# Kernel tuning notes

Hardware: AMD Instinct MI355X
Metric: run time of the kernel (lower is better)

## Reference

```python
import jax, jax.numpy as jnp
import numpy as np

HEADS = 8
HID = 128
N_A = 10000
N_B = 10000
E = 120000
NG = 8  # graphs in batch
F_A = 256
F_B = 128
NEG_SLOPE = 0.2


def _gat(h_src, h_dst, src, dst, ws, wd, a_s, a_d, bias, num_dst):
    """PyG GATConv, bipartite, concat=False, add_self_loops=False."""
    hs = (h_src @ ws).reshape(-1, HEADS, HID)   # [N_src, H, C]
    hd = (h_dst @ wd).reshape(-1, HEADS, HID)   # [N_dst, H, C]
    al_s = jnp.sum(hs * a_s, axis=-1)           # [N_src, H]
    al_d = jnp.sum(hd * a_d, axis=-1)           # [N_dst, H]
    e = jax.nn.leaky_relu(al_s[src] + al_d[dst], NEG_SLOPE)  # [E, H]
    m = jax.ops.segment_max(e, dst, num_segments=num_dst)
    ex = jnp.exp(e - m[dst])
    denom = jax.ops.segment_sum(ex, dst, num_segments=num_dst)
    alpha = ex / (denom[dst] + 1e-16)           # segment softmax over in-edges
    msg = hs[src] * alpha[:, :, None]           # [E, H, C]
    out = jax.ops.segment_sum(msg, dst, num_segments=num_dst)
    return out.mean(axis=1) + bias              # concat=False -> head mean + bias


def _mean_pool(x, batch, num_graphs):
    s = jax.ops.segment_sum(x, batch, num_segments=num_graphs)
    cnt = jax.ops.segment_sum(jnp.ones((x.shape[0],), x.dtype), batch, num_segments=num_graphs)
    return s / jnp.maximum(cnt, 1.0)[:, None]


def setup_inputs() -> dict:
    key = jax.random.key(0)
    ks = iter(jax.random.split(key, 48))
    rn = lambda shape, s=0.05: jax.random.normal(next(ks), shape, jnp.float32) * s
    inp = {
        'x_a': jax.random.normal(next(ks), (N_A, F_A), jnp.float32),
        'x_b': jax.random.normal(next(ks), (N_B, F_B), jnp.float32),
        'edge_ab': jax.random.randint(next(ks), (2, E), 0, N_A, jnp.int32),
        'edge_ba': jax.random.randint(next(ks), (2, E), 0, N_B, jnp.int32),
        'batch_a': jnp.sort(jax.random.randint(next(ks), (N_A,), 0, NG, jnp.int32)),
        'batch_b': jnp.sort(jax.random.randint(next(ks), (N_B,), 0, NG, jnp.int32)),
        'lin_a_w': rn((F_A, HID)), 'lin_a_b': rn((HID,)),
        'lin_b_w': rn((F_B, HID)), 'lin_b_b': rn((HID,)),
        'fc_w': rn((2 * HID, 1)), 'fc_b': rn((1,)),
    }
    for layer in ('1', '2'):
        for rel in ('ab', 'ba'):
            inp[f'w{layer}s_{rel}'] = rn((HID, HEADS * HID))
            inp[f'w{layer}d_{rel}'] = rn((HID, HEADS * HID))
            inp[f'a{layer}s_{rel}'] = rn((HEADS, HID))
            inp[f'a{layer}d_{rel}'] = rn((HEADS, HID))
            inp[f'b{layer}_{rel}'] = rn((HID,))
    return inp


def reference(x_a, x_b, edge_ab, edge_ba, batch_a, batch_b,
              lin_a_w, lin_a_b, lin_b_w, lin_b_b, fc_w, fc_b,
              w1s_ab, w1d_ab, a1s_ab, a1d_ab, b1_ab,
              w1s_ba, w1d_ba, a1s_ba, a1d_ba, b1_ba,
              w2s_ab, w2d_ab, a2s_ab, a2d_ab, b2_ab,
              w2s_ba, w2d_ba, a2s_ba, a2d_ba, b2_ba):
    ha = jax.nn.relu(x_a @ lin_a_w + lin_a_b)
    hb = jax.nn.relu(x_b @ lin_b_w + lin_b_b)
    # layer 1 (each dst type receives exactly one relation -> HeteroConv mean is identity)
    hb1 = _gat(ha, hb, edge_ab[0], edge_ab[1], w1s_ab, w1d_ab, a1s_ab, a1d_ab, b1_ab, N_B)
    ha1 = _gat(hb, ha, edge_ba[0], edge_ba[1], w1s_ba, w1d_ba, a1s_ba, a1d_ba, b1_ba, N_A)
    ha1 = jax.nn.relu(ha1)
    hb1 = jax.nn.relu(hb1)
    # layer 2
    hb2 = _gat(ha1, hb1, edge_ab[0], edge_ab[1], w2s_ab, w2d_ab, a2s_ab, a2d_ab, b2_ab, N_B)
    ha2 = _gat(hb1, ha1, edge_ba[0], edge_ba[1], w2s_ba, w2d_ba, a2s_ba, a2d_ba, b2_ba, N_A)
    pa = _mean_pool(ha2, batch_a, NG)
    pb = _mean_pool(hb2, batch_b, NG)
    g = jnp.concatenate([pa, pb], axis=1)       # [NG, 2*HID]
    return (g @ fc_w + fc_b).squeeze(-1)        # [NG]
```

## Files before the change

### kernel.cpp

```cpp
#include <hip/hip_runtime.h>
#include <math.h>

#define HID 128
#define HEADS 8

typedef __attribute__((ext_vector_type(8))) short s16x8;
typedef __attribute__((ext_vector_type(4))) float f32x4;

__device__ __forceinline__ unsigned short bf16_rne(float x) {
  unsigned u = __float_as_uint(x);
  unsigned r = u + 0x7FFFu + ((u >> 16) & 1u);
  return (unsigned short)(r >> 16);
}
__device__ __forceinline__ float bf16f(unsigned short h) {
  return __uint_as_float(((unsigned)h) << 16);
}

struct PrepArgs {
  const float* W[8];
  const float* a[8];
  unsigned short* WThi[4];
  unsigned short* WTlo[4];
  float* v[8];
};
struct PrepX {
  const float* lwa; const float* lwb;
  unsigned short *wa_hi, *wa_lo, *wb_hi, *wb_lo;
  int KA, KB, nwa, nwb;
};

__global__ __launch_bounds__(256) void prep_hist(
    PrepArgs p, PrepX px,
    const int* __restrict__ dst_ab, const int* __restrict__ dst_ba,
    int* __restrict__ cnt_ab, int* __restrict__ cnt_ba, int E)
{
  int bid = blockIdx.x;
  if (bid < 2048) {
    int g = bid >> 9;
    int idx = ((bid & 511) << 8) + threadIdx.x;
    int kidx = idx & 1023;
    int c = idx >> 10;
    int h = kidx >> 7, k = kidx & 127;
    float wv = p.W[2 * g][(size_t)k * (HEADS * HID) + h * HID + c];
    unsigned short hi = bf16_rne(wv);
    unsigned short lo = bf16_rne(wv - bf16f(hi));
    p.WThi[g][idx] = hi;
    p.WTlo[g][idx] = lo;
  } else if (bid < 2080) {
    int u = bid - 2048;
    int wi = u >> 2;
    int gid = ((u & 3) << 8) + threadIdx.x;
    int k = gid >> 3, h = gid & 7;
    const float* wr = p.W[wi] + (size_t)k * (HEADS * HID) + h * HID;
    const float* ar = p.a[wi] + (size_t)h * HID;
    float s = 0.f;
    for (int c = 0; c < HID; c++) s = fmaf(wr[c], ar[c], s);
    p.v[wi][gid] = s;
  } else if (bid < 2080 + px.nwa) {
    int idx = (bid - 2080) * 256 + threadIdx.x;
    if (idx < px.KA * HID) {
      int k = idx % px.KA, c = idx / px.KA;
      float wv = px.lwa[(size_t)k * HID + c];
      unsigned short hi = bf16_rne(wv);
      unsigned short lo = bf16_rne(wv - bf16f(hi));
      px.wa_hi[idx] = hi;
      px.wa_lo[idx] = lo;
    }
  } else if (bid < 2080 + px.nwa + px.nwb) {
    int idx = (bid - 2080 - px.nwa) * 256 + threadIdx.x;
    if (idx < px.KB * HID) {
      int k = idx % px.KB, c = idx / px.KB;
      float wv = px.lwb[(size_t)k * HID + c];
      unsigned short hi = bf16_rne(wv);
      unsigned short lo = bf16_rne(wv - bf16f(hi));
      px.wb_hi[idx] = hi;
      px.wb_lo[idx] = lo;
    }
  } else {
    int gid = (bid - 2080 - px.nwa - px.nwb) * 256 + threadIdx.x;
    if (gid < E) atomicAdd(&cnt_ab[dst_ab[gid]], 1);
    else if (gid < 2 * E) atomicAdd(&cnt_ba[dst_ba[gid - E]], 1);
  }
}

__global__ __launch_bounds__(1024) void scan2(
    const int* __restrict__ cnt_ab, const int* __restrict__ cnt_ba,
    int* __restrict__ ip_ab, int* __restrict__ ip_ba, int n_ab, int n_ba)
{
  const int* cnt = (blockIdx.x == 0) ? cnt_ab : cnt_ba;
  int* indptr = (blockIdx.x == 0) ? ip_ab : ip_ba;
  int n = (blockIdx.x == 0) ? n_ab : n_ba;
  __shared__ int parts[1024];
  const int tid = threadIdx.x;
  const int base = tid * 10;
  int local[10];
  int s = 0;
#pragma unroll
  for (int j = 0; j < 10; j++) {
    int v = (base + j < n) ? cnt[base + j] : 0;
    local[j] = v; s += v;
  }
  parts[tid] = s;
  __syncthreads();
  for (int off = 1; off < 1024; off <<= 1) {
    int v = (tid >= off) ? parts[tid - off] : 0;
    __syncthreads();
    parts[tid] += v;
    __syncthreads();
  }
  int ex = parts[tid] - s;
#pragma unroll
  for (int j = 0; j < 10; j++) {
    if (base + j < n) indptr[base + j] = ex;
    ex += local[j];
  }
  if (tid == 1023) indptr[n] = parts[1023];
}

__global__ __launch_bounds__(256) void scatter2(
    const int* __restrict__ edge_ab, const int* __restrict__ edge_ba,
    const int* __restrict__ ip_ab, const int* __restrict__ ip_ba,
    int* __restrict__ cur_ab, int* __restrict__ cur_ba,
    int* __restrict__ srcs_ab, int* __restrict__ srcs_ba, int E)
{
  int gid = blockIdx.x * 256 + threadIdx.x;
  if (gid < E) {
    int d = edge_ab[E + gid];
    int pos = ip_ab[d] + atomicAdd(&cur_ab[d], 1);
    srcs_ab[pos] = edge_ab[gid];
  } else if (gid < 2 * E) {
    int g = gid - E;
    int d = edge_ba[E + g];
    int pos = ip_ba[d] + atomicAdd(&cur_ba[d], 1);
    srcs_ba[pos] = edge_ba[g];
  }
}

struct ISeg {
  const float* A;
  const unsigned short* Bhi; const unsigned short* Blo;
  float* out; const float* bias; int M; int K; int yb;
};

__global__ __launch_bounds__(256) void gemm_mfma_in(ISeg s0, ISeg s1)
{
  __shared__ __align__(16) unsigned short smem[12288];
  const int tid = threadIdx.x;
  const float* A; const unsigned short *Bhi, *Blo; const float* bias; float* out;
  int M, K, ytile;
  if ((int)blockIdx.x < s0.yb) {
    A = s0.A; Bhi = s0.Bhi; Blo = s0.Blo; out = s0.out; bias = s0.bias;
    M = s0.M; K = s0.K; ytile = blockIdx.x;
  } else {
    A = s1.A; Bhi = s1.Bhi; Blo = s1.Blo; out = s1.out; bias = s1.bias;
    M = s1.M; K = s1.K; ytile = blockIdx.x - s0.yb;
  }
  const int bm = ytile * 64;
  const int nks = K >> 5;

  const int sr = tid >> 2;
  const int sg = tid & 3;
  const int g1 = sg ^ ((sr >> 1) & 3);
  const int sr2 = sr + 64;
  const int g2 = sg ^ ((sr2 >> 1) & 3);
  const int aslot  = sr * 32 + g1 * 8;
  const int bslotA = sr * 32 + g1 * 8;
  const int bslotB = sr2 * 32 + g2 * 8;
  const int gr = bm + sr;
  const bool arow_ok = (gr < M);
  const float* gA = A + (size_t)gr * K + sg * 8;
  const unsigned short* gB0 = Bhi + (size_t)sr  * K + sg * 8;
  const unsigned short* gB1 = Bhi + (size_t)sr2 * K + sg * 8;
  const unsigned short* gC0 = Blo + (size_t)sr  * K + sg * 8;
  const unsigned short* gC1 = Blo + (size_t)sr2 * K + sg * 8;

  const int l = tid & 63;
  const int w = tid >> 6;
  const int kg = l >> 4;
  int aoff[4], boff[2];
#pragma unroll
  for (int mi = 0; mi < 4; mi++) {
    int r = mi * 16 + (l & 15);
    aoff[mi] = r * 32 + (kg ^ ((r >> 1) & 3)) * 8;
  }
#pragma unroll
  for (int ni = 0; ni < 2; ni++) {
    int r = w * 32 + ni * 16 + (l & 15);
    boff[ni] = r * 32 + (kg ^ ((r >> 1) & 3)) * 8;
  }

  f32x4 acc[4][2];
  const f32x4 z4 = {0.f, 0.f, 0.f, 0.f};
#pragma unroll
  for (int mi = 0; mi < 4; mi++)
#pragma unroll
    for (int ni = 0; ni < 2; ni++) acc[mi][ni] = z4;

  float4 fa0 = make_float4(0.f, 0.f, 0.f, 0.f), fa1 = fa0;
  if (arow_ok) { fa0 = *(const float4*)gA; fa1 = *(const float4*)(gA + 4); }
  uint4 rB0 = *(const uint4*)gB0;
  uint4 rB1 = *(const uint4*)gB1;
  uint4 rC0 = *(const uint4*)gC0;
  uint4 rC1 = *(const uint4*)gC1;

  for (int ks = 0; ks < nks; ks++) {
    {
      const float f[8] = {fa0.x, fa0.y, fa0.z, fa0.w, fa1.x, fa1.y, fa1.z, fa1.w};
      unsigned au[4], lu[4];
#pragma unroll
      for (int i = 0; i < 4; i++) {
        unsigned short h0 = bf16_rne(f[2 * i]);
        unsigned short l0 = bf16_rne(f[2 * i] - bf16f(h0));
        unsigned short h1 = bf16_rne(f[2 * i + 1]);
        unsigned short l1 = bf16_rne(f[2 * i + 1] - bf16f(h1));
        au[i] = (unsigned)h0 | ((unsigned)h1 << 16);
        lu[i] = (unsigned)l0 | ((unsigned)l1 << 16);
      }
      *(uint4*)&smem[aslot]        = make_uint4(au[0], au[1], au[2], au[3]);
      *(uint4*)&smem[2048 + aslot] = make_uint4(lu[0], lu[1], lu[2], lu[3]);
    }
    *(uint4*)&smem[4096 + bslotA] = rB0;
    *(uint4*)&smem[4096 + bslotB] = rB1;
    *(uint4*)&smem[8192 + bslotA] = rC0;
    *(uint4*)&smem[8192 + bslotB] = rC1;
    __syncthreads();
    if (ks < nks - 1) {
      const int k0 = (ks + 1) * 32;
      if (arow_ok) {
        fa0 = *(const float4*)(gA + k0);
        fa1 = *(const float4*)(gA + k0 + 4);
      }
      rB0 = *(const uint4*)(gB0 + k0);
      rB1 = *(const uint4*)(gB1 + k0);
      rC0 = *(const uint4*)(gC0 + k0);
      rC1 = *(const uint4*)(gC1 + k0);
    }
    s16x8 bh0 = *(const s16x8*)&smem[4096 + boff[0]];
    s16x8 bh1 = *(const s16x8*)&smem[4096 + boff[1]];
    s16x8 bl0 = *(const s16x8*)&smem[8192 + boff[0]];
    s16x8 bl1 = *(const s16x8*)&smem[8192 + boff[1]];
#pragma unroll
    for (int mi = 0; mi < 4; mi++) {
      s16x8 ah = *(const s16x8*)&smem[aoff[mi]];
      s16x8 al = *(const s16x8*)&smem[2048 + aoff[mi]];
      acc[mi][0] = __builtin_amdgcn_mfma_f32_16x16x32_bf16(ah, bh0, acc[mi][0], 0, 0, 0);
      acc[mi][1] = __builtin_amdgcn_mfma_f32_16x16x32_bf16(ah, bh1, acc[mi][1], 0, 0, 0);
      acc[mi][0] = __builtin_amdgcn_mfma_f32_16x16x32_bf16(ah, bl0, acc[mi][0], 0, 0, 0);
      acc[mi][1] = __builtin_amdgcn_mfma_f32_16x16x32_bf16(ah, bl1, acc[mi][1], 0, 0, 0);
      acc[mi][0] = __builtin_amdgcn_mfma_f32_16x16x32_bf16(al, bh0, acc[mi][0], 0, 0, 0);
      acc[mi][1] = __builtin_amdgcn_mfma_f32_16x16x32_bf16(al, bh1, acc[mi][1], 0, 0, 0);
      acc[mi][0] = __builtin_amdgcn_mfma_f32_16x16x32_bf16(al, bl0, acc[mi][0], 0, 0, 0);
      acc[mi][1] = __builtin_amdgcn_mfma_f32_16x16x32_bf16(al, bl1, acc[mi][1], 0, 0, 0);
    }
    __syncthreads();
  }

  const int q = l >> 4, cl = l & 15;
#pragma unroll
  for (int ni = 0; ni < 2; ni++) {
    const int col = w * 32 + ni * 16 + cl;
    const float bv = bias[col];
#pragma unroll
    for (int mi = 0; mi < 4; mi++) {
      const int r0 = bm + mi * 16 + q * 4;
      const f32x4 v = acc[mi][ni];
#pragma unroll
      for (int j = 0; j < 4; j++) {
        const int r = r0 + j;
        if (r < M) {
          float x = v[j] + bv;
          x = fmaxf(x, 0.f);
          out[(size_t)r * HID + col] = x;
        }
      }
    }
  }
}

__global__ __launch_bounds__(256) void compute_al4(
    const float* __restrict__ ha, const float* __restrict__ hb,
    const float* __restrict__ v4,
    float* __restrict__ o0, float* __restrict__ o1,
    float* __restrict__ o2, float* __restrict__ o3, int na, int nb)
{
  __shared__ float vsh[4 * HID * HEADS];
  for (int i = threadIdx.x; i < 4 * HID * HEADS; i += 256) vsh[i] = v4[i];
  __syncthreads();
  int gid = blockIdx.x * 256 + threadIdx.x;
  int row = gid >> 3, h = gid & 7;
  const float* hr; float* o; int q, rl;
  if (row < na)                    { q = 0; rl = row;               hr = ha; o = o0; }
  else if (row < na + nb)          { q = 1; rl = row - na;          hr = hb; o = o1; }
  else if (row < na + 2 * nb)      { q = 2; rl = row - na - nb;     hr = hb; o = o2; }
  else if (row < 2 * na + 2 * nb)  { q = 3; rl = row - na - 2 * nb; hr = ha; o = o3; }
  else return;
  hr += (size_t)rl * HID;
  const float* vq = vsh + q * HID * HEADS;
  float s = 0.f;
  for (int k = 0; k < HID; k++) s = fmaf(hr[k], vq[k * HEADS + h], s);
  o[(size_t)rl * HEADS + h] = s;
}

struct GDir {
  const int* indptr; const int* srcs;
  const float* als; const float* ald;
  const float* h;
  unsigned short* zhi; unsigned short* zlo;
};

__global__ __launch_bounds__(256) void gat_edge2(GDir d0, GDir d1, int n0, int ntot)
{
  const int w = threadIdx.x >> 6;
  const int lane = threadIdx.x & 63;
  const int g = blockIdx.x * 4 + w;
  if (g >= ntot) return;
  const bool first = (g < n0);
  const int n = first ? g : g - n0;
  const int* indptr = first ? d0.indptr : d1.indptr;
  const int* srcs   = first ? d0.srcs   : d1.srcs;
  const float* als  = first ? d0.als    : d1.als;
  const float* ald  = first ? d0.ald    : d1.ald;
  const float* hsrc = first ? d0.h      : d1.h;
  unsigned short* zh = (first ? d0.zhi : d1.zhi) + (size_t)n * (HEADS * HID);
  unsigned short* zl = (first ? d0.zlo : d1.zlo) + (size_t)n * (HEADS * HID);

  const int base = indptr[n];
  const int deg = indptr[n + 1] - base;
  if (deg == 0) {
#pragma unroll
    for (int hh = 0; hh < HEADS; hh++) {
      *(unsigned*)(zh + hh * HID + 2 * lane) = 0u;
      *(unsigned*)(zl + hh * HID + 2 * lane) = 0u;
    }
    return;
  }
  const int eh = lane >> 3, h = lane & 7;
  const float aldn = ald[(size_t)n * HEADS + h];
  const int nch = (deg + 7) >> 3;
  const int ncc = nch < 4 ? nch : 4;

  int sc[4];
  float vc[4];
#pragma unroll
  for (int c = 0; c < 4; c++) {
    int e = c * 8 + eh;
    sc[c] = (c < ncc && e < deg) ? srcs[base + e] : -1;
  }
#pragma unroll
  for (int c = 0; c < 4; c++)
    vc[c] = (sc[c] >= 0) ? als[(size_t)sc[c] * HEADS + h] : 0.f;
  float den = 0.f;
#pragma unroll
  for (int c = 0; c < 4; c++) {
    float v = vc[c] + aldn;
    v = v > 0.f ? v : 0.2f * v;
    float ex = (sc[c] >= 0) ? expf(v) : 0.f;
    vc[c] = ex;
    den += ex;
  }
  for (int e0 = 32; e0 < deg; e0 += 8) {
    int e = e0 + eh;
    if (e < deg) {
      int s = srcs[base + e];
      float v = als[(size_t)s * HEADS + h] + aldn;
      v = v > 0.f ? v : 0.2f * v;
      den += expf(v);
    }
  }
  den += __shfl_xor(den, 8);
  den += __shfl_xor(den, 16);
  den += __shfl_xor(den, 32);

  float acc[16];
#pragma unroll
  for (int i = 0; i < 16; i++) acc[i] = 0.f;
#pragma unroll
  for (int c = 0; c < 4; c++) {
    if (c >= ncc) break;
    const int rem = deg - c * 8;
    const int elim = rem < 8 ? rem : 8;
#pragma unroll
    for (int half = 0; half < 2; half++) {
      if (half * 4 >= elim) break;
      int sj[4];
#pragma unroll
      for (int j = 0; j < 4; j++) {
        int s = __shfl(sc[c], (half * 4 + j) * 8);
        sj[j] = s < 0 ? 0 : s;
      }
      float2 hv[4];
#pragma unroll
      for (int j = 0; j < 4; j++)
        hv[j] = *(const float2*)(hsrc + (size_t)sj[j] * HID + 2 * lane);
#pragma unroll
      for (int j = 0; j < 4; j++) {
#pragma unroll
        for (int hh = 0; hh < 8; hh++) {
          float a = __shfl(vc[c], (half * 4 + j) * 8 + hh);
          acc[2 * hh]     = fmaf(a, hv[j].x, acc[2 * hh]);
          acc[2 * hh + 1] = fmaf(a, hv[j].y, acc[2 * hh + 1]);
        }
      }
    }
  }
  for (int e0 = 32; e0 < deg; e0 += 8) {
    int e = e0 + eh;
    int s = (e < deg) ? srcs[base + e] : -1;
    float ex = 0.f;
    if (s >= 0) {
      float v = als[(size_t)s * HEADS + h] + aldn;
      v = v > 0.f ? v : 0.2f * v;
      ex = expf(v);
    }
    int elim = deg - e0; if (elim > 8) elim = 8;
    for (int e8 = 0; e8 < elim; e8++) {
      int ss = __shfl(s, e8 * 8);
      const float2 hvt = *(const float2*)(hsrc + (size_t)ss * HID + 2 * lane);
#pragma unroll
      for (int hh = 0; hh < 8; hh++) {
        float a = __shfl(ex, e8 * 8 + hh);
        acc[2 * hh]     = fmaf(a, hvt.x, acc[2 * hh]);
        acc[2 * hh + 1] = fmaf(a, hvt.y, acc[2 * hh + 1]);
      }
    }
  }
#pragma unroll
  for (int hh = 0; hh < 8; hh++) {
    float dh = __shfl(den, hh);
    float inv = 1.f / (dh + 1e-16f);
    float x0 = acc[2 * hh] * inv;
    float x1 = acc[2 * hh + 1] * inv;
    unsigned short h0 = bf16_rne(x0), h1 = bf16_rne(x1);
    unsigned short l0 = bf16_rne(x0 - bf16f(h0)), l1 = bf16_rne(x1 - bf16f(h1));
    *(unsigned*)(zh + hh * HID + 2 * lane) = (unsigned)h0 | ((unsigned)h1 << 16);
    *(unsigned*)(zl + hh * HID + 2 * lane) = (unsigned)l0 | ((unsigned)l1 << 16);
  }
}

struct MSeg {
  const unsigned short* Ahi; const unsigned short* Alo;
  const unsigned short* Bhi; const unsigned short* Blo;
  float* out; const float* bias; int M; int yb;
};

__global__ __launch_bounds__(512) void gemm_mfma8(MSeg s0, MSeg s1, float scale, int do_relu)
{
  __shared__ __align__(16) unsigned short smem[24576];
  const int tid = threadIdx.x;
  const unsigned short *Ahi, *Alo, *Bhi, *Blo; const float* bias; float* out; int M, ytile;
  if ((int)blockIdx.x < s0.yb) {
    Ahi = s0.Ahi; Alo = s0.Alo; Bhi = s0.Bhi; Blo = s0.Blo;
    out = s0.out; bias = s0.bias; M = s0.M; ytile = blockIdx.x;
  } else {
    Ahi = s1.Ahi; Alo = s1.Alo; Bhi = s1.Bhi; Blo = s1.Blo;
    out = s1.out; bias = s1.bias; M = s1.M; ytile = blockIdx.x - s0.yb;
  }
  const int bm = ytile * 64;
  const int half = tid >> 8;
  const int t = tid & 255;
  const int kbase = half * 512;
  unsigned short* sm = smem + half * 12288;

  const int sr = t >> 2;
  const int sg = t & 3;
  const int g1 = sg ^ ((sr >> 1) & 3);
  const int sr2 = sr + 64;
  const int g2 = sg ^ ((sr2 >> 1) & 3);
  const int aslot  = sr * 32 + g1 * 8;
  const int bslotA = sr * 32 + g1 * 8;
  const int bslotB = sr2 * 32 + g2 * 8;
  const unsigned short* gA  = Ahi + (size_t)(bm + sr) * 1024 + kbase + sg * 8;
  const unsigned short* gAl = Alo + (size_t)(bm + sr) * 1024 + kbase + sg * 8;
  const unsigned short* gB0 = Bhi + (size_t)sr  * 1024 + kbase + sg * 8;
  const unsigned short* gB1 = Bhi + (size_t)sr2 * 1024 + kbase + sg * 8;
  const unsigned short* gC0 = Blo + (size_t)sr  * 1024 + kbase + sg * 8;
  const unsigned short* gC1 = Blo + (size_t)sr2 * 1024 + kbase + sg * 8;

  const int l = t & 63;
  const int w = t >> 6;
  const int kg = l >> 4;
  int aoff[4], boff[2];
#pragma unroll
  for (int mi = 0; mi < 4; mi++) {
    int r = mi * 16 + (l & 15);
    aoff[mi] = r * 32 + (kg ^ ((r >> 1) & 3)) * 8;
  }
#pragma unroll
  for (int ni = 0; ni < 2; ni++) {
    int r = w * 32 + ni * 16 + (l & 15);
    boff[ni] = r * 32 + (kg ^ ((r >> 1) & 3)) * 8;
  }

  f32x4 acc[4][2];
  const f32x4 z4 = {0.f, 0.f, 0.f, 0.f};
#pragma unroll
  for (int mi = 0; mi < 4; mi++)
#pragma unroll
    for (int ni = 0; ni < 2; ni++) acc[mi][ni] = z4;

  uint4 rA  = *(const uint4*)gA;
  uint4 rAl = *(const uint4*)gAl;
  uint4 rB0 = *(const uint4*)gB0;
  uint4 rB1 = *(const uint4*)gB1;
  uint4 rC0 = *(const uint4*)gC0;
  uint4 rC1 = *(const uint4*)gC1;

  for (int ks = 0; ks < 16; ks++) {
    *(uint4*)&sm[aslot]         = rA;
    *(uint4*)&sm[2048 + aslot]  = rAl;
    *(uint4*)&sm[4096 + bslotA] = rB0;
    *(uint4*)&sm[4096 + bslotB] = rB1;
    *(uint4*)&sm[8192 + bslotA] = rC0;
    *(uint4*)&sm[8192 + bslotB] = rC1;
    __syncthreads();
    if (ks < 15) {
      const int k0 = (ks + 1) * 32;
      rA  = *(const uint4*)(gA  + k0);
      rAl = *(const uint4*)(gAl + k0);
      rB0 = *(const uint4*)(gB0 + k0);
      rB1 = *(const uint4*)(gB1 + k0);
      rC0 = *(const uint4*)(gC0 + k0);
      rC1 = *(const uint4*)(gC1 + k0);
    }
    s16x8 bh0 = *(const s16x8*)&sm[4096 + boff[0]];
    s16x8 bh1 = *(const s16x8*)&sm[4096 + boff[1]];
    s16x8 bl0 = *(const s16x8*)&sm[8192 + boff[0]];
    s16x8 bl1 = *(const s16x8*)&sm[8192 + boff[1]];
#pragma unroll
    for (int mi = 0; mi < 4; mi++) {
      s16x8 ah = *(const s16x8*)&sm[aoff[mi]];
      s16x8 al = *(const s16x8*)&sm[2048 + aoff[mi]];
      acc[mi][0] = __builtin_amdgcn_mfma_f32_16x16x32_bf16(ah, bh0, acc[mi][0], 0, 0, 0);
      acc[mi][1] = __builtin_amdgcn_mfma_f32_16x16x32_bf16(ah, bh1, acc[mi][1], 0, 0, 0);
      acc[mi][0] = __builtin_amdgcn_mfma_f32_16x16x32_bf16(ah, bl0, acc[mi][0], 0, 0, 0);
      acc[mi][1] = __builtin_amdgcn_mfma_f32_16x16x32_bf16(ah, bl1, acc[mi][1], 0, 0, 0);
      acc[mi][0] = __builtin_amdgcn_mfma_f32_16x16x32_bf16(al, bh0, acc[mi][0], 0, 0, 0);
      acc[mi][1] = __builtin_amdgcn_mfma_f32_16x16x32_bf16(al, bh1, acc[mi][1], 0, 0, 0);
      acc[mi][0] = __builtin_amdgcn_mfma_f32_16x16x32_bf16(al, bl0, acc[mi][0], 0, 0, 0);
      acc[mi][1] = __builtin_amdgcn_mfma_f32_16x16x32_bf16(al, bl1, acc[mi][1], 0, 0, 0);
    }
    __syncthreads();
  }

  float* fred = (float*)smem;
  const int q = l >> 4, cl = l & 15;
  if (half == 1) {
#pragma unroll
    for (int ni = 0; ni < 2; ni++) {
      const int col = w * 32 + ni * 16 + cl;
#pragma unroll
      for (int mi = 0; mi < 4; mi++) {
        const f32x4 v = acc[mi][ni];
#pragma unroll
        for (int j = 0; j < 4; j++)
          fred[(mi * 16 + q * 4 + j) * 128 + col] = v[j];
      }
    }
  }
  __syncthreads();
  if (half == 0) {
#pragma unroll
    for (int ni = 0; ni < 2; ni++) {
      const int col = w * 32 + ni * 16 + cl;
      const float bv = bias[col];
#pragma unroll
      for (int mi = 0; mi < 4; mi++) {
        const int rt = mi * 16 + q * 4;
        const f32x4 v = acc[mi][ni];
#pragma unroll
        for (int j = 0; j < 4; j++) {
          const int r = bm + rt + j;
          if (r < M) {
            float x = (v[j] + fred[(rt + j) * 128 + col]) * scale + bv;
            if (do_relu) x = fmaxf(x, 0.f);
            out[(size_t)r * HID + col] = x;
          }
        }
      }
    }
  }
}

__global__ __launch_bounds__(256) void pool_fin(
    const float* __restrict__ ha, const float* __restrict__ hb,
    const int* __restrict__ batch_a, const int* __restrict__ batch_b,
    const float* __restrict__ fc_w, const float* __restrict__ fc_b,
    float* __restrict__ gsum, int* __restrict__ ticket,
    float* __restrict__ out, int na, int nb, int ng)
{
  const bool isA = blockIdx.x < 160;
  const float* h = isA ? ha : hb;
  const int* batch = isA ? batch_a : batch_b;
  const float* wseg = isA ? fc_w : fc_w + HID;
  float* gs = isA ? gsum : gsum + 8;
  const int n = isA ? na : nb;
  const int b = isA ? blockIdx.x : blockIdx.x - 160;

  __shared__ float sg[8];
  __shared__ int lastf;
  if (threadIdx.x < 8) sg[threadIdx.x] = 0.f;
  __syncthreads();
  const int lane = threadIdx.x & 63;
  const int wv = threadIdx.x >> 6;
  const int gw = b * 4 + wv;
  const int tw = 160 * 4;
  const float2 w2 = *(const float2*)(wseg + lane * 2);
  for (int r = gw; r < n; r += tw) {
    float2 hv = *(const float2*)(h + (size_t)r * HID + lane * 2);
    float s = hv.x * w2.x + hv.y * w2.y;
#pragma unroll
    for (int off = 32; off > 0; off >>= 1) s += __shfl_down(s, off, 64);
    if (lane == 0) atomicAdd(&sg[batch[r]], s);
  }
  __syncthreads();
  if (threadIdx.x < 8) atomicAdd(&gs[threadIdx.x], sg[threadIdx.x]);
  if (threadIdx.x == 0) {
    __threadfence();
    int tk = atomicAdd(ticket, 1);
    lastf = (tk == (int)gridDim.x - 1);
  }
  __syncthreads();
  if (lastf) {
    int g = threadIdx.x;
    if (g < ng) {
      int l, r, lo;
      l = 0; r = na; while (l < r) { int m = (l + r) >> 1; if (batch_a[m] < g) l = m + 1; else r = m; } lo = l;
      r = na; while (l < r) { int m = (l + r) >> 1; if (batch_a[m] < g + 1) l = m + 1; else r = m; }
      int ca = l - lo; if (ca < 1) ca = 1;
      l = 0; r = nb; while (l < r) { int m = (l + r) >> 1; if (batch_b[m] < g) l = m + 1; else r = m; } lo = l;
      r = nb; while (l < r) { int m = (l + r) >> 1; if (batch_b[m] < g + 1) l = m + 1; else r = m; }
      int cb = l - lo; if (cb < 1) cb = 1;
      float va = atomicAdd(&gsum[g], 0.f);
      float vb = atomicAdd(&gsum[8 + g], 0.f);
      out[g] = va / (float)ca + vb / (float)cb + fc_b[0];
    }
  }
}

extern "C" void kernel_launch(void* const* d_in, const int* in_sizes, int n_in,
                              void* d_out, int out_size, void* d_ws, size_t ws_size,
                              hipStream_t stream)
{
  const float* x_a = (const float*)d_in[0];
  const float* x_b = (const float*)d_in[1];
  const int* edge_ab = (const int*)d_in[2];
  const int* edge_ba = (const int*)d_in[3];
  const int* batch_a = (const int*)d_in[4];
  const int* batch_b = (const int*)d_in[5];
  const float* lin_a_w = (const float*)d_in[6];
  const float* lin_a_b = (const float*)d_in[7];
  const float* lin_b_w = (const float*)d_in[8];
  const float* lin_b_b = (const float*)d_in[9];
  const float* fc_w = (const float*)d_in[10];
  const float* fc_b = (const float*)d_in[11];

  const int NA = in_sizes[4];
  const int NB = in_sizes[5];
  const int E  = in_sizes[2] / 2;
  const int FA = in_sizes[0] / NA;
  const int FB = in_sizes[1] / NB;
  const int NG = out_size;
  const int NMAX = NA > NB ? NA : NB;
  const int NAp = (NA + 127) & ~127, NBp = (NB + 127) & ~127;
  const int NMAXp = NAp > NBp ? NAp : NBp;

  auto al256 = [](size_t b) { return (b + 255) & ~(size_t)255; };
  size_t fixed = 0;
  fixed += 3 * al256((size_t)NAp * HID * 4) + 3 * al256((size_t)NBp * HID * 4);
  fixed += 2 * al256((size_t)NMAXp * 1024 * 2);
  fixed += al256((size_t)8 * 131072 * 2);
  fixed += 2 * al256((size_t)FA * HID * 2) + 2 * al256((size_t)FB * HID * 2);
  fixed += al256((size_t)8 * HID * HEADS * 4);
  fixed += 2 * al256((size_t)NAp * HEADS * 4) + 2 * al256((size_t)NBp * HEADS * 4);
  fixed += al256(((size_t)4 * NMAX + 24) * 4);
  fixed += al256((size_t)(NB + 1) * 4) + al256((size_t)(NA + 1) * 4);
  fixed += 2 * al256((size_t)E * 4);
  fixed += 8192;
  const size_t zba_sz = 2 * al256((size_t)NAp * 1024 * 2);

  bool dual = (fixed + zba_sz <= ws_size);
  if (fixed > ws_size) return;

  char* w = (char*)d_ws;
  auto carve = [&](size_t bytes) -> void* {
    void* p = (void*)w;
    w += (bytes + 255) & ~(size_t)255;
    return p;
  };
  float* ha0 = (float*)carve((size_t)NAp * HID * 4);
  float* hb0 = (float*)carve((size_t)NBp * HID * 4);
  float* ha1 = (float*)carve((size_t)NAp * HID * 4);
  float* hb1 = (float*)carve((size_t)NBp * HID * 4);
  float* ha2 = (float*)carve((size_t)NAp * HID * 4);
  float* hb2 = (float*)carve((size_t)NBp * HID * 4);
  unsigned short* zab_hi = (unsigned short*)carve((size_t)NMAXp * 1024 * 2);
  unsigned short* zab_lo = (unsigned short*)carve((size_t)NMAXp * 1024 * 2);
  unsigned short* zba_hi = dual ? (unsigned short*)carve((size_t)NAp * 1024 * 2) : zab_hi;
  unsigned short* zba_lo = dual ? (unsigned short*)carve((size_t)NAp * 1024 * 2) : zab_lo;
  unsigned short* WT = (unsigned short*)carve((size_t)8 * 131072 * 2);
  unsigned short* wa_hi = (unsigned short*)carve((size_t)FA * HID * 2);
  unsigned short* wa_lo = (unsigned short*)carve((size_t)FA * HID * 2);
  unsigned short* wb_hi = (unsigned short*)carve((size_t)FB * HID * 2);
  unsigned short* wb_lo = (unsigned short*)carve((size_t)FB * HID * 2);
  float* vv  = (float*)carve((size_t)8 * HID * HEADS * 4);
  float* als_ab = (float*)carve((size_t)NAp * HEADS * 4);
  float* ald_ab = (float*)carve((size_t)NBp * HEADS * 4);
  float* als_ba = (float*)carve((size_t)NBp * HEADS * 4);
  float* ald_ba = (float*)carve((size_t)NAp * HEADS * 4);
  int* csrblk = (int*)carve(((size_t)4 * NMAX + 24) * 4);
  int* indptr_ab = (int*)carve((size_t)(NB + 1) * 4);
  int* indptr_ba = (int*)carve((size_t)(NA + 1) * 4);
  int* srcs_ab   = (int*)carve((size_t)E * 4);
  int* srcs_ba   = (int*)carve((size_t)E * 4);
  if ((size_t)(w - (char*)d_ws) > ws_size) return;

  int* cnt_ab = csrblk;
  int* cnt_ba = csrblk + NMAX;
  int* cur_ab = csrblk + 2 * NMAX;
  int* cur_ba = csrblk + 3 * NMAX;
  float* gsum = (float*)(csrblk + 4 * NMAX);
  int* ticket = csrblk + 4 * NMAX + 16;

  hipMemsetAsync(csrblk, 0, ((size_t)4 * NMAX + 24) * 4, stream);

  PrepArgs pa;
  const int wi_idx[8] = {12, 13, 17, 18, 22, 23, 27, 28};
  const int ai_idx[8] = {14, 15, 19, 20, 24, 25, 29, 30};
  for (int i = 0; i < 8; i++) {
    pa.W[i] = (const float*)d_in[wi_idx[i]];
    pa.a[i] = (const float*)d_in[ai_idx[i]];
    pa.v[i] = vv + (size_t)i * HID * HEADS;
  }
  for (int g = 0; g < 4; g++) {
    pa.WThi[g] = WT + (size_t)g * 131072;
    pa.WTlo[g] = WT + (size_t)(4 + g) * 131072;
  }
  PrepX px;
  px.lwa = lin_a_w; px.lwb = lin_b_w;
  px.wa_hi = wa_hi; px.wa_lo = wa_lo; px.wb_hi = wb_hi; px.wb_lo = wb_lo;
  px.KA = FA; px.KB = FB;
  px.nwa = (FA * HID + 255) / 256;
  px.nwb = (FB * HID + 255) / 256;
  const int hist_b = (2 * E + 255) / 256;
  prep_hist<<<2080 + px.nwa + px.nwb + hist_b, 256, 0, stream>>>(
      pa, px, edge_ab + E, edge_ba + E, cnt_ab, cnt_ba, E);
  scan2<<<2, 1024, 0, stream>>>(cnt_ab, cnt_ba, indptr_ab, indptr_ba, NB, NA);
  scatter2<<<(2 * E + 255) / 256, 256, 0, stream>>>(
      edge_ab, edge_ba, indptr_ab, indptr_ba, cur_ab, cur_ba, srcs_ab, srcs_ba, E);

  {
    ISeg sa = {x_a, wa_hi, wa_lo, ha0, lin_a_b, NA, FA, NAp / 64};
    ISeg sb = {x_b, wb_hi, wb_lo, hb0, lin_b_b, NB, FB, NBp / 64};
    gemm_mfma_in<<<NAp / 64 + NBp / 64, 256, 0, stream>>>(sa, sb);
  }

  auto run_layer = [&](int L, const float* haP, const float* hbP,
                       float* haN, float* hbN, const float* b_ab, const float* b_ba,
                       int relu) {
    compute_al4<<<((2 * (NA + NB)) * HEADS + 255) / 256, 256, 0, stream>>>(
        haP, hbP, vv + (size_t)L * 4 * HID * HEADS,
        als_ab, ald_ab, als_ba, ald_ba, NA, NB);
    GDir dab = {indptr_ab, srcs_ab, als_ab, ald_ab, haP, zab_hi, zab_lo};
    GDir dba = {indptr_ba, srcs_ba, als_ba, ald_ba, hbP, zba_hi, zba_lo};
    const int gab = 2 * L, gba = 2 * L + 1;
    MSeg mab = {zab_hi, zab_lo, WT + (size_t)gab * 131072, WT + (size_t)(4 + gab) * 131072,
                hbN, b_ab, NB, NBp / 64};
    MSeg mba = {zba_hi, zba_lo, WT + (size_t)gba * 131072, WT + (size_t)(4 + gba) * 131072,
                haN, b_ba, NA, NAp / 64};
    if (dual) {
      gat_edge2<<<(NB + NA + 3) / 4, 256, 0, stream>>>(dab, dba, NB, NB + NA);
      gemm_mfma8<<<NBp / 64 + NAp / 64, 512, 0, stream>>>(mab, mba, 1.f / HEADS, relu);
    } else {
      MSeg mz = {nullptr, nullptr, nullptr, nullptr, nullptr, nullptr, 0, 0};
      gat_edge2<<<(NB + 3) / 4, 256, 0, stream>>>(dab, dab, NB, NB);
      gemm_mfma8<<<NBp / 64, 512, 0, stream>>>(mab, mz, 1.f / HEADS, relu);
      gat_edge2<<<(NA + 3) / 4, 256, 0, stream>>>(dba, dba, NA, NA);
      gemm_mfma8<<<NAp / 64, 512, 0, stream>>>(mba, mz, 1.f / HEADS, relu);
    }
  };

  run_layer(0, ha0, hb0, ha1, hb1, (const float*)d_in[16], (const float*)d_in[21], 1);
  run_layer(1, ha1, hb1, ha2, hb2, (const float*)d_in[26], (const float*)d_in[31], 0);

  pool_fin<<<320, 256, 0, stream>>>(ha2, hb2, batch_a, batch_b, fc_w, fc_b,
                                    gsum, ticket, (float*)d_out, NA, NB, NG);
}
```

Baseline: 371.9 us.

## Split the post-aggregation GEMM along K with a separate reduce-and-epilogue kernel

The fused 512-thread GEMM, which split K in two halves inside a block and reduced through shared memory, becomes a 256-thread split-K kernel. It uses a grid dimension of KS (up to 4) slices that write fp32 partials to a workspace buffer, and a new reduce_epi kernel sums the partials and applies scale, bias and ReLU. The aim is more blocks in flight and better occupancy, since the old grid had only about 320 blocks. The cost is an extra kernel launch per layer plus the round trip of the partials through global memory, and the workspace requirement grows, so the code now picks KS based on available workspace.

```diff
diff --git a/kernel.cpp b/kernel.cpp
--- a/kernel.cpp
+++ b/kernel.cpp
@@ -440,44 +440,44 @@
 struct MSeg {
   const unsigned short* Ahi; const unsigned short* Alo;
   const unsigned short* Bhi; const unsigned short* Blo;
-  float* out; const float* bias; int M; int yb;
+  int M; int yb;
 };
 
-__global__ __launch_bounds__(512) void gemm_mfma8(MSeg s0, MSeg s1, float scale, int do_relu)
-{
-  __shared__ __align__(16) unsigned short smem[24576];
+__global__ __launch_bounds__(256, 2) void gemm_mfma_splitk(
+    MSeg s0, MSeg s1, float* __restrict__ P, int Mtot, int KS)
+{
+  __shared__ __align__(16) unsigned short smem[12288];
   const int tid = threadIdx.x;
-  const unsigned short *Ahi, *Alo, *Bhi, *Blo; const float* bias; float* out; int M, ytile;
+  const unsigned short *Ahi, *Alo, *Bhi, *Blo; int M, ytile, rowbase;
   if ((int)blockIdx.x < s0.yb) {
     Ahi = s0.Ahi; Alo = s0.Alo; Bhi = s0.Bhi; Blo = s0.Blo;
-    out = s0.out; bias = s0.bias; M = s0.M; ytile = blockIdx.x;
+    M = s0.M; ytile = blockIdx.x; rowbase = 0;
   } else {
     Ahi = s1.Ahi; Alo = s1.Alo; Bhi = s1.Bhi; Blo = s1.Blo;
-    out = s1.out; bias = s1.bias; M = s1.M; ytile = blockIdx.x - s0.yb;
+    M = s1.M; ytile = blockIdx.x - s0.yb; rowbase = s0.yb * 64;
   }
   const int bm = ytile * 64;
-  const int half = tid >> 8;
-  const int t = tid & 255;
-  const int kbase = half * 512;
-  unsigned short* sm = smem + half * 12288;
-
-  const int sr = t >> 2;
-  const int sg = t & 3;
+  const int kchunk = 1024 / KS;
+  const int kbeg = blockIdx.y * kchunk;
+  const int nks = kchunk / 32;
+
+  const int sr = tid >> 2;
+  const int sg = tid & 3;
   const int g1 = sg ^ ((sr >> 1) & 3);
   const int sr2 = sr + 64;
   const int g2 = sg ^ ((sr2 >> 1) & 3);
   const int aslot  = sr * 32 + g1 * 8;
   const int bslotA = sr * 32 + g1 * 8;
   const int bslotB = sr2 * 32 + g2 * 8;
-  const unsigned short* gA  = Ahi + (size_t)(bm + sr) * 1024 + kbase + sg * 8;
-  const unsigned short* gAl = Alo + (size_t)(bm + sr) * 1024 + kbase + sg * 8;
-  const unsigned short* gB0 = Bhi + (size_t)sr  * 1024 + kbase + sg * 8;
-  const unsigned short* gB1 = Bhi + (size_t)sr2 * 1024 + kbase + sg * 8;
-  const unsigned short* gC0 = Blo + (size_t)sr  * 1024 + kbase + sg * 8;
-  const unsigned short* gC1 = Blo + (size_t)sr2 * 1024 + kbase + sg * 8;
-
-  const int l = t & 63;
-  const int w = t >> 6;
+  const unsigned short* gA  = Ahi + (size_t)(bm + sr) * 1024 + kbeg + sg * 8;
+  const unsigned short* gAl = Alo + (size_t)(bm + sr) * 1024 + kbeg + sg * 8;
+  const unsigned short* gB0 = Bhi + (size_t)sr  * 1024 + kbeg + sg * 8;
+  const unsigned short* gB1 = Bhi + (size_t)sr2 * 1024 + kbeg + sg * 8;
+  const unsigned short* gC0 = Blo + (size_t)sr  * 1024 + kbeg + sg * 8;
+  const unsigned short* gC1 = Blo + (size_t)sr2 * 1024 + kbeg + sg * 8;
+
+  const int l = tid & 63;
+  const int w = tid >> 6;
   const int kg = l >> 4;
   int aoff[4], boff[2];
 #pragma unroll
@@ -505,15 +505,15 @@
   uint4 rC0 = *(const uint4*)gC0;
   uint4 rC1 = *(const uint4*)gC1;
 
-  for (int ks = 0; ks < 16; ks++) {
-    *(uint4*)&sm[aslot]         = rA;
-    *(uint4*)&sm[2048 + aslot]  = rAl;
-    *(uint4*)&sm[4096 + bslotA] = rB0;
-    *(uint4*)&sm[4096 + bslotB] = rB1;
-    *(uint4*)&sm[8192 + bslotA] = rC0;
-    *(uint4*)&sm[8192 + bslotB] = rC1;
+  for (int ks = 0; ks < nks; ks++) {
+    *(uint4*)&smem[aslot]         = rA;
+    *(uint4*)&smem[2048 + aslot]  = rAl;
+    *(uint4*)&smem[4096 + bslotA] = rB0;
+    *(uint4*)&smem[4096 + bslotB] = rB1;
+    *(uint4*)&smem[8192 + bslotA] = rC0;
+    *(uint4*)&smem[8192 + bslotB] = rC1;
     __syncthreads();
-    if (ks < 15) {
+    if (ks < nks - 1) {
       const int k0 = (ks + 1) * 32;
       rA  = *(const uint4*)(gA  + k0);
       rAl = *(const uint4*)(gAl + k0);
@@ -522,14 +522,14 @@
       rC0 = *(const uint4*)(gC0 + k0);
       rC1 = *(const uint4*)(gC1 + k0);
     }
-    s16x8 bh0 = *(const s16x8*)&sm[4096 + boff[0]];
-    s16x8 bh1 = *(const s16x8*)&sm[4096 + boff[1]];
-    s16x8 bl0 = *(const s16x8*)&sm[8192 + boff[0]];
-    s16x8 bl1 = *(const s16x8*)&sm[8192 + boff[1]];
+    s16x8 bh0 = *(const s16x8*)&smem[4096 + boff[0]];
+    s16x8 bh1 = *(const s16x8*)&smem[4096 + boff[1]];
+    s16x8 bl0 = *(const s16x8*)&smem[8192 + boff[0]];
+    s16x8 bl1 = *(const s16x8*)&smem[8192 + boff[1]];
 #pragma unroll
     for (int mi = 0; mi < 4; mi++) {
-      s16x8 ah = *(const s16x8*)&sm[aoff[mi]];
-      s16x8 al = *(const s16x8*)&sm[2048 + aoff[mi]];
+      s16x8 ah = *(const s16x8*)&smem[aoff[mi]];
+      s16x8 al = *(const s16x8*)&smem[2048 + aoff[mi]];
       acc[mi][0] = __builtin_amdgcn_mfma_f32_16x16x32_bf16(ah, bh0, acc[mi][0], 0, 0, 0);
       acc[mi][1] = __builtin_amdgcn_mfma_f32_16x16x32_bf16(ah, bh1, acc[mi][1], 0, 0, 0);
       acc[mi][0] = __builtin_amdgcn_mfma_f32_16x16x32_bf16(ah, bl0, acc[mi][0], 0, 0, 0);
@@ -542,43 +542,57 @@
     __syncthreads();
   }
 
-  float* fred = (float*)smem;
   const int q = l >> 4, cl = l & 15;
-  if (half == 1) {
-#pragma unroll
-    for (int ni = 0; ni < 2; ni++) {
-      const int col = w * 32 + ni * 16 + cl;
-#pragma unroll
-      for (int mi = 0; mi < 4; mi++) {
-        const f32x4 v = acc[mi][ni];
-#pragma unroll
-        for (int j = 0; j < 4; j++)
-          fred[(mi * 16 + q * 4 + j) * 128 + col] = v[j];
+  const size_t prow0 = (size_t)blockIdx.y * Mtot + rowbase + bm;
+#pragma unroll
+  for (int ni = 0; ni < 2; ni++) {
+    const int col = w * 32 + ni * 16 + cl;
+#pragma unroll
+    for (int mi = 0; mi < 4; mi++) {
+      const int r0 = mi * 16 + q * 4;
+      const f32x4 v = acc[mi][ni];
+#pragma unroll
+      for (int j = 0; j < 4; j++) {
+        const int r = r0 + j;
+        if (bm + r < M) P[(prow0 + r) * HID + col] = v[j];
       }
     }
   }
-  __syncthreads();
-  if (half == 0) {
-#pragma unroll
-    for (int ni = 0; ni < 2; ni++) {
-      const int col = w * 32 + ni * 16 + cl;
-      const float bv = bias[col];
-#pragma unroll
-      for (int mi = 0; mi < 4; mi++) {
-        const int rt = mi * 16 + q * 4;
-        const f32x4 v = acc[mi][ni];
-#pragma unroll
-        for (int j = 0; j < 4; j++) {
-          const int r = bm + rt + j;
-          if (r < M) {
-            float x = (v[j] + fred[(rt + j) * 128 + col]) * scale + bv;
-            if (do_relu) x = fmaxf(x, 0.f);
-            out[(size_t)r * HID + col] = x;
-          }
-        }
-      }
-    }
-  }
+}
+
+struct RSeg { float* out; const float* bias; int M; int rowbase; };
+
+__global__ __launch_bounds__(256) void reduce_epi(
+    const float* __restrict__ P, int Mtot, int KS, float scale, int do_relu,
+    RSeg s0, RSeg s1)
+{
+  int idx = blockIdx.x * 256 + threadIdx.x;
+  if (idx >= Mtot * 32) return;
+  int r = idx >> 5;
+  int c = (idx & 31) << 2;
+  float* outp; const float* bias; int rl;
+  if (s1.M > 0 && r >= s1.rowbase) {
+    rl = r - s1.rowbase; if (rl >= s1.M) return; outp = s1.out; bias = s1.bias;
+  } else {
+    rl = r; if (rl >= s0.M) return; outp = s0.out; bias = s0.bias;
+  }
+  float4 acc = make_float4(0.f, 0.f, 0.f, 0.f);
+  for (int z = 0; z < KS; z++) {
+    const float4 v = *(const float4*)(P + ((size_t)z * Mtot + r) * HID + c);
+    acc.x += v.x; acc.y += v.y; acc.z += v.z; acc.w += v.w;
+  }
+  const float4 b = *(const float4*)(bias + c);
+  acc.x = acc.x * scale + b.x;
+  acc.y = acc.y * scale + b.y;
+  acc.z = acc.z * scale + b.z;
+  acc.w = acc.w * scale + b.w;
+  if (do_relu) {
+    acc.x = acc.x > 0.f ? acc.x : 0.f;
+    acc.y = acc.y > 0.f ? acc.y : 0.f;
+    acc.z = acc.z > 0.f ? acc.z : 0.f;
+    acc.w = acc.w > 0.f ? acc.w : 0.f;
+  }
+  *(float4*)(outp + (size_t)rl * HID + c) = acc;
 }
 
 __global__ __launch_bounds__(256) void pool_fin(
@@ -663,6 +677,7 @@
   const int NMAX = NA > NB ? NA : NB;
   const int NAp = (NA + 127) & ~127, NBp = (NB + 127) & ~127;
   const int NMAXp = NAp > NBp ? NAp : NBp;
+  const int Mtot = NAp + NBp;
 
   auto al256 = [](size_t b) { return (b + 255) & ~(size_t)255; };
   size_t fixed = 0;
@@ -677,9 +692,15 @@
   fixed += 2 * al256((size_t)E * 4);
   fixed += 8192;
   const size_t zba_sz = 2 * al256((size_t)NAp * 1024 * 2);
-
-  bool dual = (fixed + zba_sz <= ws_size);
-  if (fixed > ws_size) return;
+  const size_t pslice = al256((size_t)Mtot * HID * 4);
+
+  int KS = 4; bool dual = true;
+  if (fixed + zba_sz + 4 * pslice <= ws_size)      { dual = true;  KS = 4; }
+  else if (fixed + zba_sz + 2 * pslice <= ws_size) { dual = true;  KS = 2; }
+  else if (fixed + 4 * pslice <= ws_size)          { dual = false; KS = 4; }
+  else if (fixed + 2 * pslice <= ws_size)          { dual = false; KS = 2; }
+  else if (fixed + 1 * pslice <= ws_size)          { dual = false; KS = 1; }
+  else return;
 
   char* w = (char*)d_ws;
   auto carve = [&](size_t bytes) -> void* {
@@ -697,6 +718,7 @@
   unsigned short* zab_lo = (unsigned short*)carve((size_t)NMAXp * 1024 * 2);
   unsigned short* zba_hi = dual ? (unsigned short*)carve((size_t)NAp * 1024 * 2) : zab_hi;
   unsigned short* zba_lo = dual ? (unsigned short*)carve((size_t)NAp * 1024 * 2) : zab_lo;
+  float* P = (float*)carve((size_t)KS * Mtot * HID * 4);
   unsigned short* WT = (unsigned short*)carve((size_t)8 * 131072 * 2);
   unsigned short* wa_hi = (unsigned short*)carve((size_t)FA * HID * 2);
   unsigned short* wa_lo = (unsigned short*)carve((size_t)FA * HID * 2);
@@ -754,6 +776,9 @@
     gemm_mfma_in<<<NAp / 64 + NBp / 64, 256, 0, stream>>>(sa, sb);
   }
 
+  const int red_grid = (Mtot * 32 + 255) / 256;
+  const RSeg rnone = {nullptr, nullptr, 0, 0};
+
   auto run_layer = [&](int L, const float* haP, const float* hbP,
                        float* haN, float* hbN, const float* b_ab, const float* b_ba,
                        int relu) {
@@ -764,18 +789,25 @@
     GDir dba = {indptr_ba, srcs_ba, als_ba, ald_ba, hbP, zba_hi, zba_lo};
     const int gab = 2 * L, gba = 2 * L + 1;
     MSeg mab = {zab_hi, zab_lo, WT + (size_t)gab * 131072, WT + (size_t)(4 + gab) * 131072,
-                hbN, b_ab, NB, NBp / 64};
+                NB, NBp / 64};
     MSeg mba = {zba_hi, zba_lo, WT + (size_t)gba * 131072, WT + (size_t)(4 + gba) * 131072,
-                haN, b_ba, NA, NAp / 64};
+                NA, NAp / 64};
     if (dual) {
       gat_edge2<<<(NB + NA + 3) / 4, 256, 0, stream>>>(dab, dba, NB, NB + NA);
-      gemm_mfma8<<<NBp / 64 + NAp / 64, 512, 0, stream>>>(mab, mba, 1.f / HEADS, relu);
+      gemm_mfma_splitk<<<dim3(NBp / 64 + NAp / 64, KS), 256, 0, stream>>>(mab, mba, P, Mtot, KS);
+      RSeg r0 = {hbN, b_ab, NB, 0};
+      RSeg r1 = {haN, b_ba, NA, NBp};
+      reduce_epi<<<red_grid, 256, 0, stream>>>(P, Mtot, KS, 1.f / HEADS, relu, r0, r1);
     } else {
-      MSeg mz = {nullptr, nullptr, nullptr, nullptr, nullptr, nullptr, 0, 0};
+      MSeg mz = {nullptr, nullptr, nullptr, nullptr, 0, 0};
       gat_edge2<<<(NB + 3) / 4, 256, 0, stream>>>(dab, dab, NB, NB);
-      gemm_mfma8<<<NBp / 64, 512, 0, stream>>>(mab, mz, 1.f / HEADS, relu);
+      gemm_mfma_splitk<<<dim3(NBp / 64, KS), 256, 0, stream>>>(mab, mz, P, NBp, KS);
+      RSeg r0 = {hbN, b_ab, NB, 0};
+      reduce_epi<<<(NBp * 32 + 255) / 256, 256, 0, stream>>>(P, NBp, KS, 1.f / HEADS, relu, r0, rnone);
       gat_edge2<<<(NA + 3) / 4, 256, 0, stream>>>(dba, dba, NA, NA);
-      gemm_mfma8<<<NAp / 64, 512, 0, stream>>>(mba, mz, 1.f / HEADS, relu);
+      gemm_mfma_splitk<<<dim3(NAp / 64, KS), 256, 0, stream>>>(mba, mz, P, NAp, KS);
+      RSeg r1 = {haN, b_ba, NA, 0};
+      reduce_epi<<<(NAp * 32 + 255) / 256, 256, 0, stream>>>(P, NAp, KS, 1.f / HEADS, relu, r1, rnone);
     }
   };
 
```

New measurement: 370.4 us. About the same (-0.4%).
